# Kernel optimization log

Measured on AMD Instinct MI355X. Metric: run time of the kernel, lower is better.

Reference implementation:

```python
import jax, jax.numpy as jnp
import numpy as np

ALPHA = 10.0
BETA = 2.0
BASE = 0.5
BIG = 1e9


def setup_inputs() -> dict:
    key = jax.random.key(0)
    k1, k2, k3 = jax.random.split(key, 3)
    n, d, n_cls = 8192, 1024, 512
    x = jax.random.normal(k1, (n, d), dtype=jnp.float32)
    x = x / jnp.linalg.norm(x, axis=1, keepdims=True)  # metric-learning embeddings are L2-normalized
    targets = jax.random.randint(k2, (n,), 0, n_cls, dtype=jnp.int64)
    margin = jax.random.uniform(k3, (n,), dtype=jnp.float32) * 0.1
    return {"inputs": x, "targets": targets, "margin": margin}


def reference(inputs, targets, margin):
    n = inputs.shape[0]
    sim = jnp.matmul(inputs, inputs.T)  # [n, n]
    same = targets[:, None] == targets[None, :]
    pos_mask = same & (sim < 1.0)          # masked_select(targets==t_i) then (< 1)
    neg_mask = ~same
    # sort()[0] / sort()[-1] -> per-row min of positives, max of negatives
    min_pos = jnp.min(jnp.where(pos_mask, sim, BIG), axis=1)   # [n]
    max_neg = jnp.max(jnp.where(neg_mask, sim, -BIG), axis=1)  # [n]
    m = margin[:, None]
    # hard mining: relu-threshold then recover original sim values
    keep_neg = neg_mask & ((sim + m - min_pos[:, None]) > 0)
    keep_pos = pos_mask & ((max_neg[:, None] - sim + m) > 0)
    ap = jnp.sum(keep_pos, axis=1)
    an = jnp.sum(keep_neg, axis=1)
    valid = (ap > 0) & (an > 0)
    pos_loss = (2.0 / BETA) * jnp.log1p(
        jnp.sum(jnp.where(keep_pos, jnp.exp(-BETA * (sim - BASE)), 0.0), axis=1))
    neg_loss = (2.0 / ALPHA) * jnp.log1p(
        jnp.sum(jnp.where(keep_neg, jnp.exp(ALPHA * (sim - BASE)), 0.0), axis=1))
    loss = jnp.sum(jnp.where(valid, pos_loss + neg_loss, 0.0)) / n
    anchor = valid.astype(jnp.int32)
    ap_out = jnp.where(valid, ap, 0).astype(jnp.int32)
    an_out = jnp.where(valid, an, 0).astype(jnp.int32)
    total = jnp.sum(ap_out) + jnp.sum(an_out)
    return (loss, anchor, ap_out, an_out, total)
```

## Files before the change

kernel.cpp:

```cpp
#include <hip/hip_runtime.h>
#include <math.h>

#define N_ROWS 8192
#define DIMS   1024
#define NCLS   512
#define BK     32
#define NQ     64
#define NWG2   1056
#define CA     14

typedef __attribute__((ext_vector_type(8))) short bf16x8;
typedef __attribute__((ext_vector_type(4))) float f32x4;
typedef unsigned long long ull;

__device__ __forceinline__ unsigned short f2bf(float f) {
    unsigned u = __float_as_uint(f);
    u += 0x7FFFu + ((u >> 16) & 1u);
    return (unsigned short)(u >> 16);
}
__device__ __forceinline__ float bf2f(unsigned short h) {
    return __uint_as_float(((unsigned)h) << 16);
}
__device__ __forceinline__ unsigned enc_f(float x) {
    unsigned u = __float_as_uint(x);
    return (u & 0x80000000u) ? ~u : (u | 0x80000000u);
}
__device__ __forceinline__ float dec_f(unsigned u) {
    return (u & 0x80000000u) ? __uint_as_float(u ^ 0x80000000u) : __uint_as_float(~u);
}

__device__ __forceinline__ float dot1024(const float* __restrict__ xi,
                                         const float* __restrict__ xj) {
    const float4* u4 = (const float4*)xi;
    const float4* v4 = (const float4*)xj;
    float a0 = 0.f, a1 = 0.f, a2 = 0.f, a3 = 0.f;
#pragma unroll 8
    for (int q = 0; q < DIMS / 4; ++q) {
        float4 u = u4[q], v = v4[q];
        a0 += u.x * v.x; a1 += u.y * v.y;
        a2 += u.z * v.z; a3 += u.w * v.w;
    }
    return (a0 + a1) + (a2 + a3);
}

typedef __attribute__((address_space(1))) const void* as1_cvp;
typedef __attribute__((address_space(3))) void* as3_vp;
__device__ __forceinline__ void gl_lds16(const void* g, void* l) {
    __builtin_amdgcn_global_load_lds((as1_cvp)g, (as3_vp)l, 16, 0, 0);
}

__global__ __launch_bounds__(256) void setup_k(const float* __restrict__ X,
                                               const int* __restrict__ raw,
                                               short* __restrict__ Xhi,
                                               short* __restrict__ Xlo,
                                               float* __restrict__ sumsq,
                                               int* __restrict__ tgt,
                                               int* __restrict__ cnt,
                                               int* __restrict__ offs,
                                               int* __restrict__ pairoff,
                                               int* __restrict__ members,
                                               int* __restrict__ an_cnt,
                                               float* __restrict__ neg_sum,
                                               ull* __restrict__ maxneg,
                                               float* __restrict__ out,
                                               int simcap) {
    __shared__ int sflag;
    __shared__ int scnt[NCLS], soff[NCLS], spair[NCLS], scur[NCLS];
    __shared__ int schunk[16], schunkp[16];
    int tid = threadIdx.x;

    if (blockIdx.x == 0) {
        if (tid == 0) { sflag = 0; out[0] = 0.f; out[1 + 3 * N_ROWS] = 0.f; }
        for (int c = tid; c < NCLS; c += 256) scnt[c] = 0;
        __syncthreads();
        int any = 0;
        for (int i = tid; i < N_ROWS / 2; i += 256) any |= raw[2 * i + 1];
        if (any) atomicOr(&sflag, 1);
        __syncthreads();
        int is32 = sflag;
        for (int i = tid; i < N_ROWS; i += 256) {
            int t = is32 ? raw[i] : raw[2 * i];
            tgt[i] = t;
            if ((unsigned)t < NCLS) atomicAdd(&scnt[t], 1);
        }
        __syncthreads();
        if (tid < 16) {
            int s = 0, sp = 0;
            for (int c = tid * 32; c < tid * 32 + 32; ++c) {
                int k = scnt[c]; int kk = k < 256 ? k : 256;
                s += k; sp += kk * kk;
            }
            schunk[tid] = s; schunkp[tid] = sp;
        }
        __syncthreads();
        if (tid == 0) {
            int s = 0, sp = 0;
            for (int t = 0; t < 16; ++t) {
                int a = schunk[t], b = schunkp[t];
                schunk[t] = s; schunkp[t] = sp;
                s += a; sp += b;
            }
        }
        __syncthreads();
        if (tid < 16) {
            int s = schunk[tid], sp = schunkp[tid];
            for (int c = tid * 32; c < tid * 32 + 32; ++c) {
                int k = scnt[c]; int kk = k < 256 ? k : 256;
                soff[c] = s; scur[c] = s;
                spair[c] = (simcap > 0 && sp + kk * kk <= simcap) ? sp : -1;
                s += k; sp += kk * kk;
            }
        }
        __syncthreads();
        for (int i = tid; i < N_ROWS; i += 256) {
            int t = tgt[i];
            if ((unsigned)t < NCLS) {
                int p = atomicAdd(&scur[t], 1);
                members[p] = i;
            }
        }
        for (int c = tid; c < NCLS; c += 256) {
            cnt[c] = scnt[c]; offs[c] = soff[c]; pairoff[c] = spair[c];
        }
    } else {
        int rowbase = (blockIdx.x - 1) * 4;
        int row  = rowbase + (tid >> 6);
        int lane = tid & 63;
        const float4* xr = (const float4*)(X + (size_t)row * DIMS);
        short4* oh = (short4*)(Xhi + (size_t)row * DIMS);
        short4* ol = (short4*)(Xlo + (size_t)row * DIMS);
        float ss = 0.f;
#pragma unroll
        for (int t = 0; t < 4; ++t) {
            float4 v = xr[lane + 64 * t];
            ss += v.x * v.x + v.y * v.y + v.z * v.z + v.w * v.w;
            short4 h, l;
            unsigned short hx = f2bf(v.x); h.x = (short)hx; l.x = (short)f2bf(v.x - bf2f(hx));
            unsigned short hy = f2bf(v.y); h.y = (short)hy; l.y = (short)f2bf(v.y - bf2f(hy));
            unsigned short hz = f2bf(v.z); h.z = (short)hz; l.z = (short)f2bf(v.z - bf2f(hz));
            unsigned short hw = f2bf(v.w); h.w = (short)hw; l.w = (short)f2bf(v.w - bf2f(hw));
            oh[lane + 64 * t] = h;
            ol[lane + 64 * t] = l;
        }
#pragma unroll
        for (int off = 1; off < 64; off <<= 1) ss += __shfl_xor(ss, off);
        if (lane == 0) sumsq[row] = ss;
        if (tid < 4) {
            int r = rowbase + tid;
            an_cnt[r] = 0; neg_sum[r] = 0.f;
            maxneg[r] = ((ull)enc_f(-1e9f)) << 32;
        }
    }
}

__global__ __launch_bounds__(512) void minpos_k(const float* __restrict__ X,
                                                const int* __restrict__ members,
                                                const int* __restrict__ offs,
                                                const int* __restrict__ cnt,
                                                const int* __restrict__ pairoff,
                                                const float* __restrict__ sumsq,
                                                float* __restrict__ minpos,
                                                float* __restrict__ simbuf) {
    __shared__ __align__(16) float srows[CA][DIMS];
    __shared__ unsigned smin[256];
    int c = blockIdx.x, tid = threadIdx.x;
    int wave = tid >> 6, lane = tid & 63;
    int k = cnt[c], off = offs[c], spo = pairoff[c];
    for (int t = tid; t < 256; t += 512) smin[t] = enc_f(1e9f);
    int kk = k < 256 ? k : 256;
    __syncthreads();
    for (int a0 = 0; a0 < kk; a0 += CA) {
        int na = (kk - a0 < CA) ? (kk - a0) : CA;
        for (int idx = tid; idx < na * 256; idx += 512) {
            int r = idx >> 8, c4 = idx & 255;
            int i = members[off + a0 + r];
            ((float4*)&srows[r][0])[c4] = ((const float4*)(X + (size_t)i * DIMS))[c4];
        }
        __syncthreads();
        for (int b = wave; b < kk; b += 8) {
            int j = members[off + b];
            const float4* xj = (const float4*)(X + (size_t)j * DIMS);
            float4 rj[4];
#pragma unroll
            for (int t = 0; t < 4; ++t) rj[t] = xj[lane + 64 * t];
            int a = 0;
            for (; a + 2 <= na; a += 2) {
                int i0 = members[off + a0 + a];
                int i1 = members[off + a0 + a + 1];
                float p0 = 0.f, p1 = 0.f, p2 = 0.f, p3 = 0.f;
                float q0 = 0.f, q1 = 0.f, q2 = 0.f, q3 = 0.f;
#pragma unroll
                for (int t = 0; t < 4; ++t) {
                    float4 u0 = ((const float4*)&srows[a][0])[lane + 64 * t];
                    float4 u1 = ((const float4*)&srows[a + 1][0])[lane + 64 * t];
                    p0 += u0.x * rj[t].x; p1 += u0.y * rj[t].y;
                    p2 += u0.z * rj[t].z; p3 += u0.w * rj[t].w;
                    q0 += u1.x * rj[t].x; q1 += u1.y * rj[t].y;
                    q2 += u1.z * rj[t].z; q3 += u1.w * rj[t].w;
                }
                float s0 = (p0 + p1) + (p2 + p3);
                float s1 = (q0 + q1) + (q2 + q3);
#pragma unroll
                for (int o = 1; o < 64; o <<= 1) {
                    s0 += __shfl_xor(s0, o);
                    s1 += __shfl_xor(s1, o);
                }
                if (i0 == j) s0 = sumsq[i0];
                if (i1 == j) s1 = sumsq[i1];
                if (lane == 0) {
                    if (spo >= 0) {
                        simbuf[spo + (a0 + a) * kk + b] = s0;
                        simbuf[spo + (a0 + a + 1) * kk + b] = s1;
                    }
                    if (s0 < 1.0f) atomicMin(&smin[a0 + a], enc_f(s0));
                    if (s1 < 1.0f) atomicMin(&smin[a0 + a + 1], enc_f(s1));
                }
            }
            if (a < na) {
                int i0 = members[off + a0 + a];
                float p0 = 0.f, p1 = 0.f, p2 = 0.f, p3 = 0.f;
#pragma unroll
                for (int t = 0; t < 4; ++t) {
                    float4 u0 = ((const float4*)&srows[a][0])[lane + 64 * t];
                    p0 += u0.x * rj[t].x; p1 += u0.y * rj[t].y;
                    p2 += u0.z * rj[t].z; p3 += u0.w * rj[t].w;
                }
                float s0 = (p0 + p1) + (p2 + p3);
#pragma unroll
                for (int o = 1; o < 64; o <<= 1) s0 += __shfl_xor(s0, o);
                if (i0 == j) s0 = sumsq[i0];
                if (lane == 0) {
                    if (spo >= 0) simbuf[spo + (a0 + a) * kk + b] = s0;
                    if (s0 < 1.0f) atomicMin(&smin[a0 + a], enc_f(s0));
                }
            }
        }
        __syncthreads();
    }
    for (int a = tid; a < kk; a += 512) minpos[members[off + a]] = dec_f(smin[a]);
}

__global__ __launch_bounds__(512, 4) void fused_k(const short* __restrict__ Xhi,
                                                  const short* __restrict__ Xlo,
                                                  const int* __restrict__ tgt,
                                                  const float* __restrict__ margin,
                                                  const float* __restrict__ minpos,
                                                  ull* __restrict__ maxneg,
                                                  int* __restrict__ an_cnt,
                                                  float* __restrict__ neg_sum) {
    __shared__ __align__(16) short sAh[256][BK];
    __shared__ __align__(16) short sBh[128][BK];
    __shared__ __align__(16) short sBl[128][BK];

    int orig = blockIdx.x;
    int wgid = (orig & 7) * (NWG2 / 8) + (orig >> 3);

    int rem = wgid, p = 0;
    while (rem >= NQ - 2 * p) { rem -= NQ - 2 * p; ++p; }
    int q = 2 * p + rem;
    int row0 = p * 256, col0 = q * 128;

    int tid = threadIdx.x, lane = tid & 63, wave = tid >> 6;
    int wr = wave >> 1, wc = wave & 1;
    int l15 = lane & 15, l4 = lane >> 4;

    const short* gp[4];
    short* lp[4];
#pragma unroll
    for (int j = 0; j < 4; ++j) {
        int u = wave + 8 * j;
        const short* src; int base0, r16; short (*lb)[BK];
        if (u < 16)      { src = Xhi; base0 = row0; r16 = u * 16;        lb = sAh; }
        else if (u < 24) { src = Xhi; base0 = col0; r16 = (u - 16) * 16; lb = sBh; }
        else             { src = Xlo; base0 = col0; r16 = (u - 24) * 16; lb = sBl; }
        gp[j] = src + (size_t)(base0 + r16 + (lane >> 2)) * DIMS + (lane & 3) * 8;
        lp[j] = &lb[r16][0];
    }

    f32x4 acc[4][4] = {};

#pragma unroll 1
    for (int k0 = 0; k0 < DIMS; k0 += BK) {
        if (k0) __syncthreads();
#pragma unroll
        for (int j = 0; j < 4; ++j) gl_lds16(gp[j] + k0, lp[j]);
        __syncthreads();

        bf16x8 bh[4], bl[4];
#pragma unroll
        for (int n = 0; n < 4; ++n) {
            int rb = wc * 64 + n * 16 + l15;
            bh[n] = *(const bf16x8*)&sBh[rb][l4 * 8];
            bl[n] = *(const bf16x8*)&sBl[rb][l4 * 8];
        }
#pragma unroll
        for (int m = 0; m < 4; ++m) {
            int ra = wr * 64 + m * 16 + l15;
            bf16x8 ah = *(const bf16x8*)&sAh[ra][l4 * 8];
#pragma unroll
            for (int n = 0; n < 4; ++n) {
                acc[m][n] = __builtin_amdgcn_mfma_f32_16x16x32_bf16(ah, bh[n], acc[m][n], 0, 0, 0);
                acc[m][n] = __builtin_amdgcn_mfma_f32_16x16x32_bf16(ah, bl[n], acc[m][n], 0, 0, 0);
            }
        }
    }

    int tcol[4]; float mcol[4], pcol[4];
#pragma unroll
    for (int n = 0; n < 4; ++n) {
        int gc = col0 + wc * 64 + n * 16 + l15;
        tcol[n] = tgt[gc];
        mcol[n] = margin[gc];
        pcol[n] = minpos[gc];
    }
    ull  cmx[4] = {0, 0, 0, 0};
    float cns[4] = {0, 0, 0, 0};
    int  cct[4] = {0, 0, 0, 0};

#pragma unroll
    for (int m = 0; m < 4; ++m) {
#pragma unroll
        for (int r = 0; r < 4; ++r) {
            int grow = row0 + wr * 64 + m * 16 + l4 * 4 + r;
            int trow = tgt[grow];
            float mg = margin[grow], mp = minpos[grow];
            ull rmx = 0; float rns = 0.f; int rct = 0;
#pragma unroll
            for (int n = 0; n < 4; ++n) {
                float s = acc[m][n][r];
                int gc = col0 + wc * 64 + n * 16 + l15;
                if (trow != tcol[n] && gc > grow) {
                    float e = __expf(10.f * s - 5.f);
                    ull pk = (((ull)enc_f(s)) << 32) | (unsigned)gc;
                    rmx = rmx > pk ? rmx : pk;
                    if (s + mg - mp > 0.f) { rct++; rns += e; }
                    ull pk2 = (((ull)enc_f(s)) << 32) | (unsigned)grow;
                    cmx[n] = cmx[n] > pk2 ? cmx[n] : pk2;
                    if (s + mcol[n] - pcol[n] > 0.f) { cct[n]++; cns[n] += e; }
                }
            }
#pragma unroll
            for (int off = 1; off < 16; off <<= 1) {
                ull o = __shfl_xor(rmx, off); rmx = rmx > o ? rmx : o;
                rns += __shfl_xor(rns, off);
                rct += __shfl_xor(rct, off);
            }
            if (l15 == 0 && rmx != 0) {
                atomicMax(&maxneg[grow], rmx);
                if (rct) { atomicAdd(&an_cnt[grow], rct); atomicAdd(&neg_sum[grow], rns); }
            }
        }
    }
#pragma unroll
    for (int n = 0; n < 4; ++n) {
#pragma unroll
        for (int off = 16; off < 64; off <<= 1) {
            ull o = __shfl_xor(cmx[n], off); cmx[n] = cmx[n] > o ? cmx[n] : o;
            cns[n] += __shfl_xor(cns[n], off);
            cct[n] += __shfl_xor(cct[n], off);
        }
        if (lane < 16 && cmx[n] != 0) {
            int gc = col0 + wc * 64 + n * 16 + l15;
            atomicMax(&maxneg[gc], cmx[n]);
            if (cct[n]) { atomicAdd(&an_cnt[gc], cct[n]); atomicAdd(&neg_sum[gc], cns[n]); }
        }
    }
}

__global__ __launch_bounds__(256) void finalize_k(const float* __restrict__ X,
                                                  const int* __restrict__ members,
                                                  const int* __restrict__ offs,
                                                  const int* __restrict__ cnt,
                                                  const int* __restrict__ pairoff,
                                                  const float* __restrict__ simbuf,
                                                  const float* __restrict__ sumsq,
                                                  const float* __restrict__ margin,
                                                  const ull* __restrict__ maxneg,
                                                  const int* __restrict__ an_cnt,
                                                  const float* __restrict__ neg_sum,
                                                  float* __restrict__ out) {
    __shared__ int sap[256];
    __shared__ float sps[256];
    __shared__ float smn[256], smg[256];
    __shared__ float sred[8];
    int c = blockIdx.x, tid = threadIdx.x;
    int wave = tid >> 6, lane = tid & 63;
    int k = cnt[c], off = offs[c], spo = pairoff[c];
    int kk = k < 256 ? k : 256;
    sap[tid] = 0; sps[tid] = 0.f;

    for (int a = wave; a < kk; a += 4) {
        int i = members[off + a];
        ull pm = maxneg[i];
        float mn = -1e9f;
        if ((unsigned)(pm >> 32) != enc_f(-1e9f)) {
            int col = (int)(pm & 0xFFFFFFFFu);
            const float4* xi = (const float4*)(X + (size_t)i * DIMS);
            const float4* xj = (const float4*)(X + (size_t)col * DIMS);
            float a0 = 0.f, a1 = 0.f, a2 = 0.f, a3 = 0.f;
#pragma unroll
            for (int t = 0; t < 4; ++t) {
                float4 u = xi[lane + 64 * t], v = xj[lane + 64 * t];
                a0 += u.x * v.x; a1 += u.y * v.y;
                a2 += u.z * v.z; a3 += u.w * v.w;
            }
            float s = (a0 + a1) + (a2 + a3);
#pragma unroll
            for (int o = 1; o < 64; o <<= 1) s += __shfl_xor(s, o);
            mn = s;
        }
        if (lane == 0) { smn[a] = mn; smg[a] = margin[i]; }
    }
    __syncthreads();

    for (int p = tid; p < kk * kk; p += 256) {
        int a = p / kk;
        float s;
        if (spo >= 0) {
            s = simbuf[spo + p];
        } else {
            int b = p - a * kk;
            int i = members[off + a], j = members[off + b];
            s = (i == j) ? sumsq[i]
                         : dot1024(X + (size_t)i * DIMS, X + (size_t)j * DIMS);
        }
        if (s < 1.0f && (smn[a] - s + smg[a] > 0.f)) {
            atomicAdd(&sap[a], 1);
            atomicAdd(&sps[a], __expf(-2.f * s + 1.f));
        }
    }
    __syncthreads();

    float bl = 0.f, bt = 0.f;
    for (int a = tid; a < kk; a += 256) {
        int i = members[off + a];
        int ap = sap[a];
        int an = an_cnt[i];
        bool valid = (ap > 0) && (an > 0);
        float pl = log1pf(sps[a]);
        float nl = 0.2f * log1pf(neg_sum[i]);
        out[1 + i]              = valid ? 1.f : 0.f;
        out[1 + N_ROWS + i]     = valid ? (float)ap : 0.f;
        out[1 + 2 * N_ROWS + i] = valid ? (float)an : 0.f;
        bl += valid ? (pl + nl) : 0.f;
        bt += valid ? (float)(ap + an) : 0.f;
    }
#pragma unroll
    for (int o = 1; o < 64; o <<= 1) {
        bl += __shfl_xor(bl, o);
        bt += __shfl_xor(bt, o);
    }
    if (lane == 0) { sred[wave] = bl; sred[4 + wave] = bt; }
    __syncthreads();
    if (tid == 0) {
        float L = sred[0] + sred[1] + sred[2] + sred[3];
        float T = sred[4] + sred[5] + sred[6] + sred[7];
        atomicAdd(&out[0], L / (float)N_ROWS);
        atomicAdd(&out[1 + 3 * N_ROWS], T);
    }
}

extern "C" void kernel_launch(void* const* d_in, const int* in_sizes, int n_in,
                              void* d_out, int out_size, void* d_ws, size_t ws_size,
                              hipStream_t stream) {
    const float* X      = (const float*)d_in[0];
    const int*   rawTgt = (const int*)d_in[1];
    const float* margin = (const float*)d_in[2];
    float* out = (float*)d_out;

    char* ws = (char*)d_ws;
    short* Xhi = (short*)ws;
    short* Xlo = (short*)(ws + (size_t)16 * 1024 * 1024);
    char* p = ws + (size_t)32 * 1024 * 1024;
    float* sumsq    = (float*)p;  p += (size_t)N_ROWS * 4;
    float* minpos   = (float*)p;  p += (size_t)N_ROWS * 4;
    ull*   maxneg   = (ull*)p;    p += (size_t)N_ROWS * 8;
    int*   an_cnt   = (int*)p;    p += (size_t)N_ROWS * 4;
    float* neg_sum  = (float*)p;  p += (size_t)N_ROWS * 4;
    int*   tgt      = (int*)p;    p += (size_t)N_ROWS * 4;
    int*   members  = (int*)p;    p += (size_t)N_ROWS * 4;
    int*   cnt      = (int*)p;    p += (size_t)NCLS * 4;
    int*   offs     = (int*)p;    p += (size_t)NCLS * 4;
    int*   pairoff  = (int*)p;    p += (size_t)NCLS * 4;
    float* simbuf   = (float*)p;

    size_t used = (size_t)(p - ws);
    int simcap = (ws_size >= used + (size_t)4 * 1024 * 1024) ? (1 << 20) : 0;

    setup_k<<<1 + N_ROWS / 4, 256, 0, stream>>>(X, rawTgt, Xhi, Xlo, sumsq, tgt, cnt, offs,
                                                pairoff, members, an_cnt, neg_sum, maxneg,
                                                out, simcap);
    minpos_k<<<NCLS, 512, 0, stream>>>(X, members, offs, cnt, pairoff, sumsq, minpos, simbuf);
    fused_k<<<NWG2, 512, 0, stream>>>(Xhi, Xlo, tgt, margin, minpos, maxneg, an_cnt, neg_sum);
    finalize_k<<<NCLS, 256, 0, stream>>>(X, members, offs, cnt, pairoff, simbuf, sumsq,
                                         margin, maxneg, an_cnt, neg_sum, out);
}
```

Measured before the change: 335.7 us.

## Double-buffer LDS with BK=64 and interleave global staging with MFMA phases

The GEMM main loop of the fused kernel now uses a doubled K tile and two 64KB LDS slabs. The next tile's global-to-LDS loads are issued in four chunks interleaved with four MFMA phases, using explicit vmcnt/lgkmcnt waits, raw barriers and setprio around the MFMA bursts. The aim is to hide global load latency behind matrix math, where the old loop serialized load then compute. In exchange, LDS use grows to 128KB and launch bounds drop to one workgroup per CU, which cuts occupancy and relies on the hand-tuned wait counts being correct.

```diff
diff --git a/kernel.cpp b/kernel.cpp
--- a/kernel.cpp
+++ b/kernel.cpp
@@ -4,9 +4,11 @@
 #define N_ROWS 8192
 #define DIMS   1024
 #define NCLS   512
-#define BK     32
+#define BK     64
+#define NT     (DIMS / BK)
 #define NQ     64
 #define NWG2   1056
+#define SLABB  65536
 #define CA     14
 
 typedef __attribute__((ext_vector_type(8))) short bf16x8;
@@ -240,7 +242,29 @@
     for (int a = tid; a < kk; a += 512) minpos[members[off + a]] = dec_f(smin[a]);
 }
 
-__global__ __launch_bounds__(512, 4) void fused_k(const short* __restrict__ Xhi,
+#define VMC2 asm volatile("s_waitcnt vmcnt(2)" ::: "memory")
+#define VMC0 asm volatile("s_waitcnt vmcnt(0)" ::: "memory")
+#define LGK0 asm volatile("s_waitcnt lgkmcnt(0)" ::: "memory")
+#define BAR  __builtin_amdgcn_s_barrier()
+
+#define STAGE(u, tt, dslab)                                                        \
+    do {                                                                           \
+        gl_lds16(gpp[(u)*2 + 0] + (size_t)(tt) * BK, lds + (dslab) * SLABB + lofs[(u)*2 + 0]); \
+        gl_lds16(gpp[(u)*2 + 1] + (size_t)(tt) * BK, lds + (dslab) * SLABB + lofs[(u)*2 + 1]); \
+    } while (0)
+
+#define MFMA16(AF, BF)                                                             \
+    do {                                                                           \
+        __builtin_amdgcn_s_setprio(1);                                             \
+        _Pragma("unroll")                                                          \
+        for (int m_ = 0; m_ < 4; ++m_)                                             \
+            _Pragma("unroll")                                                      \
+            for (int n_ = 0; n_ < 4; ++n_)                                         \
+                acc[m_][n_] = __builtin_amdgcn_mfma_f32_16x16x32_bf16(AF[m_], BF[n_], acc[m_][n_], 0, 0, 0); \
+        __builtin_amdgcn_s_setprio(0);                                             \
+    } while (0)
+
+__global__ __launch_bounds__(512, 1) void fused_k(const short* __restrict__ Xhi,
                                                   const short* __restrict__ Xlo,
                                                   const int* __restrict__ tgt,
                                                   const float* __restrict__ margin,
@@ -248,9 +272,7 @@
                                                   ull* __restrict__ maxneg,
                                                   int* __restrict__ an_cnt,
                                                   float* __restrict__ neg_sum) {
-    __shared__ __align__(16) short sAh[256][BK];
-    __shared__ __align__(16) short sBh[128][BK];
-    __shared__ __align__(16) short sBl[128][BK];
+    __shared__ __align__(16) char lds[2 * SLABB];
 
     int orig = blockIdx.x;
     int wgid = (orig & 7) * (NWG2 / 8) + (orig >> 3);
@@ -264,45 +286,78 @@
     int wr = wave >> 1, wc = wave & 1;
     int l15 = lane & 15, l4 = lane >> 4;
 
-    const short* gp[4];
-    short* lp[4];
-#pragma unroll
-    for (int j = 0; j < 4; ++j) {
-        int u = wave + 8 * j;
-        const short* src; int base0, r16; short (*lb)[BK];
-        if (u < 16)      { src = Xhi; base0 = row0; r16 = u * 16;        lb = sAh; }
-        else if (u < 24) { src = Xhi; base0 = col0; r16 = (u - 16) * 16; lb = sBh; }
-        else             { src = Xlo; base0 = col0; r16 = (u - 24) * 16; lb = sBl; }
-        gp[j] = src + (size_t)(base0 + r16 + (lane >> 2)) * DIMS + (lane & 3) * 8;
-        lp[j] = &lb[r16][0];
+    const short* gpp[8];
+    int lofs[8];
+#pragma unroll
+    for (int u = 0; u < 4; ++u)
+#pragma unroll
+        for (int j = 0; j < 2; ++j) {
+            int idx = j * 512 + tid;
+            int r = idx >> 3;
+            int cs = (tid & 7) * 8;
+            const short* src = (u == 3) ? Xlo : Xhi;
+            int grow = (u == 0) ? row0 + r
+                     : (u == 1) ? row0 + 128 + r
+                                : col0 + r;
+            gpp[u * 2 + j] = src + (size_t)grow * DIMS + cs;
+            lofs[u * 2 + j] = u * 16384 + idx * 16;
+        }
+
+    int raOff[4], rbOff[4];
+#pragma unroll
+    for (int m = 0; m < 4; ++m) {
+        raOff[m] = ((wr * 64 + m * 16 + l15) << 7) + l4 * 16;
+        rbOff[m] = 32768 + ((wc * 64 + m * 16 + l15) << 7) + l4 * 16;
     }
 
     f32x4 acc[4][4] = {};
 
+#pragma unroll
+    for (int u = 0; u < 4; ++u) STAGE(u, 0, 0);
+    VMC2;
+    BAR;
+
+    int cur = 0;
 #pragma unroll 1
-    for (int k0 = 0; k0 < DIMS; k0 += BK) {
-        if (k0) __syncthreads();
-#pragma unroll
-        for (int j = 0; j < 4; ++j) gl_lds16(gp[j] + k0, lp[j]);
-        __syncthreads();
-
-        bf16x8 bh[4], bl[4];
-#pragma unroll
-        for (int n = 0; n < 4; ++n) {
-            int rb = wc * 64 + n * 16 + l15;
-            bh[n] = *(const bf16x8*)&sBh[rb][l4 * 8];
-            bl[n] = *(const bf16x8*)&sBl[rb][l4 * 8];
-        }
-#pragma unroll
-        for (int m = 0; m < 4; ++m) {
-            int ra = wr * 64 + m * 16 + l15;
-            bf16x8 ah = *(const bf16x8*)&sAh[ra][l4 * 8];
-#pragma unroll
-            for (int n = 0; n < 4; ++n) {
-                acc[m][n] = __builtin_amdgcn_mfma_f32_16x16x32_bf16(ah, bh[n], acc[m][n], 0, 0, 0);
-                acc[m][n] = __builtin_amdgcn_mfma_f32_16x16x32_bf16(ah, bl[n], acc[m][n], 0, 0, 0);
-            }
-        }
+    for (int t = 0; t < NT; ++t) {
+        char* S = lds + cur * SLABB;
+        int nxt = cur ^ 1;
+        bool stg = (t + 1 < NT);
+        bf16x8 ah[4], bh[4], bl[4];
+
+#pragma unroll
+        for (int m = 0; m < 4; ++m) ah[m] = *(const bf16x8*)(S + raOff[m]);
+#pragma unroll
+        for (int n = 0; n < 4; ++n) bh[n] = *(const bf16x8*)(S + rbOff[n]);
+        if (stg) { STAGE(0, t + 1, nxt); VMC2; } else { VMC0; }
+        BAR; LGK0;
+        MFMA16(ah, bh);
+        BAR;
+
+#pragma unroll
+        for (int n = 0; n < 4; ++n) bl[n] = *(const bf16x8*)(S + 16384 + rbOff[n]);
+        if (stg) STAGE(1, t + 1, nxt);
+        BAR; LGK0;
+        MFMA16(ah, bl);
+        BAR;
+
+#pragma unroll
+        for (int m = 0; m < 4; ++m) ah[m] = *(const bf16x8*)(S + raOff[m] + 64);
+#pragma unroll
+        for (int n = 0; n < 4; ++n) bh[n] = *(const bf16x8*)(S + rbOff[n] + 64);
+        if (stg) STAGE(2, t + 1, nxt);
+        BAR; LGK0;
+        MFMA16(ah, bh);
+        BAR;
+
+#pragma unroll
+        for (int n = 0; n < 4; ++n) bl[n] = *(const bf16x8*)(S + 16384 + rbOff[n] + 64);
+        if (stg) { STAGE(3, t + 1, nxt); VMC2; }
+        BAR; LGK0;
+        MFMA16(ah, bl);
+        BAR;
+
+        cur = nxt;
     }
 
     int tcol[4]; float mcol[4], pcol[4];
```

Measured after the change: 382.1 us. +13.8%, slower.

## Double-buffer LDS tiles in fused GEMM loop and raise MFMA priority

Applied to the files above, without the earlier changes.

Puts the A/B tiles in a single LDS array with two slabs, and prefetches the next K-slab with global-to-LDS loads while MFMAs run on the current one. Each iteration now needs one barrier instead of two. s_setprio is raised around the MFMA block, and the CA constant changes from 14 to 16. LDS use doubles, which may cut occupancy, and the overlap depends on how the loads are waited on.

```diff
diff --git a/kernel.cpp b/kernel.cpp
--- a/kernel.cpp
+++ b/kernel.cpp
@@ -5,9 +5,11 @@
 #define DIMS   1024
 #define NCLS   512
 #define BK     32
+#define NT     (DIMS / BK)
 #define NQ     64
 #define NWG2   1056
-#define CA     14
+#define SLABSH (512 * BK)
+#define CA     16
 
 typedef __attribute__((ext_vector_type(8))) short bf16x8;
 typedef __attribute__((ext_vector_type(4))) float f32x4;
@@ -248,9 +250,7 @@
                                                   ull* __restrict__ maxneg,
                                                   int* __restrict__ an_cnt,
                                                   float* __restrict__ neg_sum) {
-    __shared__ __align__(16) short sAh[256][BK];
-    __shared__ __align__(16) short sBh[128][BK];
-    __shared__ __align__(16) short sBl[128][BK];
+    __shared__ __align__(16) short lds[2 * SLABSH];
 
     int orig = blockIdx.x;
     int wgid = (orig & 7) * (NWG2 / 8) + (orig >> 3);
@@ -265,44 +265,56 @@
     int l15 = lane & 15, l4 = lane >> 4;
 
     const short* gp[4];
-    short* lp[4];
+    int lof[4];
 #pragma unroll
     for (int j = 0; j < 4; ++j) {
         int u = wave + 8 * j;
-        const short* src; int base0, r16; short (*lb)[BK];
-        if (u < 16)      { src = Xhi; base0 = row0; r16 = u * 16;        lb = sAh; }
-        else if (u < 24) { src = Xhi; base0 = col0; r16 = (u - 16) * 16; lb = sBh; }
-        else             { src = Xlo; base0 = col0; r16 = (u - 24) * 16; lb = sBl; }
+        const short* src; int base0, r16, sbase;
+        if (u < 16)      { src = Xhi; base0 = row0; r16 = u * 16;        sbase = 0; }
+        else if (u < 24) { src = Xhi; base0 = col0; r16 = (u - 16) * 16; sbase = 256 * BK; }
+        else             { src = Xlo; base0 = col0; r16 = (u - 24) * 16; sbase = 384 * BK; }
         gp[j] = src + (size_t)(base0 + r16 + (lane >> 2)) * DIMS + (lane & 3) * 8;
-        lp[j] = &lb[r16][0];
+        lof[j] = sbase + r16 * BK;
     }
 
     f32x4 acc[4][4] = {};
 
+#pragma unroll
+    for (int j = 0; j < 4; ++j) gl_lds16(gp[j], lds + lof[j]);
+    __syncthreads();
+
+    int cur = 0;
 #pragma unroll 1
-    for (int k0 = 0; k0 < DIMS; k0 += BK) {
-        if (k0) __syncthreads();
-#pragma unroll
-        for (int j = 0; j < 4; ++j) gl_lds16(gp[j] + k0, lp[j]);
-        __syncthreads();
-
+    for (int t = 0; t < NT; ++t) {
+        if (t + 1 < NT) {
+            short* ns = lds + (cur ^ 1) * SLABSH;
+#pragma unroll
+            for (int j = 0; j < 4; ++j)
+                gl_lds16(gp[j] + (size_t)(t + 1) * BK, ns + lof[j]);
+        }
+
+        short* S = lds + cur * SLABSH;
         bf16x8 bh[4], bl[4];
 #pragma unroll
         for (int n = 0; n < 4; ++n) {
             int rb = wc * 64 + n * 16 + l15;
-            bh[n] = *(const bf16x8*)&sBh[rb][l4 * 8];
-            bl[n] = *(const bf16x8*)&sBl[rb][l4 * 8];
-        }
+            bh[n] = *(const bf16x8*)(S + (256 + rb) * BK + l4 * 8);
+            bl[n] = *(const bf16x8*)(S + (384 + rb) * BK + l4 * 8);
+        }
+        __builtin_amdgcn_s_setprio(1);
 #pragma unroll
         for (int m = 0; m < 4; ++m) {
             int ra = wr * 64 + m * 16 + l15;
-            bf16x8 ah = *(const bf16x8*)&sAh[ra][l4 * 8];
+            bf16x8 ah = *(const bf16x8*)(S + ra * BK + l4 * 8);
 #pragma unroll
             for (int n = 0; n < 4; ++n) {
                 acc[m][n] = __builtin_amdgcn_mfma_f32_16x16x32_bf16(ah, bh[n], acc[m][n], 0, 0, 0);
                 acc[m][n] = __builtin_amdgcn_mfma_f32_16x16x32_bf16(ah, bl[n], acc[m][n], 0, 0, 0);
             }
         }
+        __builtin_amdgcn_s_setprio(0);
+        __syncthreads();
+        cur ^= 1;
     }
 
     int tcol[4]; float mcol[4], pcol[4];
```

After: 291.8 us. 13.1% less time.
